# Kernel tuning notes

Hardware: AMD Instinct MI355X
Metric: run time of the kernel (lower is better)

## Reference

```python
import jax, jax.numpy as jnp
import numpy as np
import math

B, T, D_MODEL, N_HEAD = 2, 2048, 1024, 16
NUM_BUCKETS, MAX_DIST = 32, 128
D_HEAD = D_MODEL // N_HEAD


def _relative_position_bucket(rel_pos, num_buckets=NUM_BUCKETS, max_distance=MAX_DIST):
    # bidirectional=True branch of the torch code
    nb = num_buckets // 2
    buckets = (rel_pos > 0).astype(jnp.int32) * nb
    rel_pos = jnp.abs(rel_pos)
    max_exact = nb // 2
    is_small = rel_pos < max_exact
    # guard log(0); masked out by is_small anyway
    large = max_exact + (
        jnp.log(jnp.maximum(rel_pos, 1).astype(jnp.float32) / max_exact)
        / math.log(max_distance / max_exact) * (nb - max_exact)
    ).astype(jnp.int32)
    large = jnp.minimum(large, nb - 1)
    return buckets + jnp.where(is_small, rel_pos, large)


def compute_bias(rel_bias, q_len, kv_len):
    qp = jnp.arange(q_len, dtype=jnp.int32)[:, None]
    kp = jnp.arange(kv_len, dtype=jnp.int32)[None, :]
    buckets = _relative_position_bucket(kp - qp)          # [Tq, Tkv]
    vals = rel_bias[buckets]                              # [Tq, Tkv, H]
    return jnp.transpose(vals, (2, 0, 1))                 # [H, Tq, Tkv]


def setup_inputs() -> dict:
    key = jax.random.key(0)
    ks = jax.random.split(key, 9)
    inp = {
        'q': jax.random.normal(ks[0], (B, T, D_MODEL), jnp.float32),
        'k': jax.random.normal(ks[1], (B, T, D_MODEL), jnp.float32),
        'v': jax.random.normal(ks[2], (B, T, D_MODEL), jnp.float32),
        'mask': jax.random.randint(ks[3], (B, T, T), 0, 2, jnp.int32),
        'Wq': jax.random.normal(ks[4], (D_MODEL, D_MODEL), jnp.float32) * 0.02,
        'Wk': jax.random.normal(ks[5], (D_MODEL, D_MODEL), jnp.float32) * 0.02,
        'Wv': jax.random.normal(ks[6], (D_MODEL, D_MODEL), jnp.float32) * 0.02,
        'Wfc': jax.random.normal(ks[7], (D_MODEL, D_MODEL), jnp.float32) * 0.02,
        'rel_bias': jax.random.normal(ks[8], (NUM_BUCKETS, N_HEAD), jnp.float32) * 0.02,
    }
    return inp


def reference(q, k, v, mask, Wq, Wk, Wv, Wfc, rel_bias):
    b, tq, _ = q.shape
    tkv = k.shape[1]
    qh = (q @ Wq).reshape(b, tq, N_HEAD, D_HEAD)
    kh = (k @ Wk).reshape(b, tkv, N_HEAD, D_HEAD)
    vh = (v @ Wv).reshape(b, tkv, N_HEAD, D_HEAD)
    attn = jnp.einsum('blhd,bthd->bhlt', qh, kh) / np.sqrt(D_HEAD).astype(np.float32)
    position_bias = compute_bias(rel_bias, tq, tkv)       # [H, Tq, Tkv]
    attn = attn + position_bias[None]                     # broadcast over batch
    attn = jnp.where(mask[:, None] == 0, -1e9, attn)
    attn = jax.nn.softmax(attn, axis=-1)                  # dropout: eval mode (identity)
    out = jnp.einsum('bhlt,bthd->blhd', attn, vh).reshape(b, tq, D_MODEL)
    out = out @ Wfc
    return out, position_bias[:, None]                    # bias returned as [H,1,Tq,Tkv] like torch
```

## Files before the change

### kernel.cpp

```cpp
#include <hip/hip_runtime.h>
#include <math.h>

#define TT 2048
#define BB 2
#define HH 16
#define DMODEL 1024
#define NREL 4095

typedef __attribute__((ext_vector_type(8)))  _Float16 half8;
typedef __attribute__((ext_vector_type(4)))  _Float16 half4;
typedef __attribute__((ext_vector_type(16))) float    f32x16;
typedef __attribute__((ext_vector_type(4)))  int      int4v;

__device__ __forceinline__ f32x16 zero16() {
    f32x16 v;
#pragma unroll
    for (int i = 0; i < 16; ++i) v[i] = 0.f;
    return v;
}

__device__ __forceinline__ unsigned pkh(float a, float b) {
    union { _Float16 h[2]; unsigned u; } x;
    x.h[0] = (_Float16)a; x.h[1] = (_Float16)b;
    return x.u;
}

__device__ __forceinline__ void gload16(const void* g, void* l) {
    __builtin_amdgcn_global_load_lds(
        (const __attribute__((address_space(1))) void*)g,
        (__attribute__((address_space(3))) void*)l, 16, 0, 0);
}

__device__ __forceinline__ int rel_bucket(int rel) {
    int base = rel > 0 ? 16 : 0;
    int r = rel < 0 ? -rel : rel;
    int lb;
    if (r < 8)       lb = r;
    else if (r < 12) lb = 8;
    else if (r < 16) lb = 9;
    else if (r < 23) lb = 10;
    else if (r < 32) lb = 11;
    else if (r < 46) lb = 12;
    else if (r < 64) lb = 13;
    else if (r < 91) lb = 14;
    else             lb = 15;
    return base + lb;
}

__global__ __launch_bounds__(256) void prep_kernel(
    const float* __restrict__ q, const float* __restrict__ k,
    const float* __restrict__ v, const int* __restrict__ mask,
    const float* __restrict__ W0, const float* __restrict__ W1,
    const float* __restrict__ W2, const float* __restrict__ W3,
    const float* __restrict__ rel_bias,
    _Float16* __restrict__ q16, _Float16* __restrict__ k16,
    _Float16* __restrict__ v16, _Float16* __restrict__ WT,
    float* __restrict__ btable, unsigned* __restrict__ mb)
{
    __shared__ float t[64][65];
    int bid = blockIdx.x, tid = threadIdx.x;
    if (bid < 256) {
        int idx = bid * 256 + tid;
        if (idx < HH * NREL) {
            int h = idx / NREL, ri = idx % NREL;
            btable[idx] = rel_bias[rel_bucket(ri - (TT - 1)) * HH + h];
        }
    } else if (bid < 1280) {
        int zz = (bid - 256) >> 8, inner = (bid - 256) & 255;
        const float* src = zz == 0 ? W0 : zz == 1 ? W1 : zz == 2 ? W2 : W3;
        _Float16* dst = WT + (size_t)zz * DMODEL * DMODEL;
        int k0 = (inner >> 4) * 64, n0 = (inner & 15) * 64;
        int r = tid >> 4, c4 = (tid & 15) * 4;
#pragma unroll
        for (int i = 0; i < 4; ++i) {
            float4 vv = *(const float4*)(src + (size_t)(k0 + r + 16 * i) * DMODEL + n0 + c4);
            t[r + 16 * i][c4] = vv.x; t[r + 16 * i][c4 + 1] = vv.y;
            t[r + 16 * i][c4 + 2] = vv.z; t[r + 16 * i][c4 + 3] = vv.w;
        }
        __syncthreads();
        int rn = tid >> 2, ck = (tid & 3) * 16;
        half8 h0, h1;
#pragma unroll
        for (int j = 0; j < 8; ++j) h0[j] = (_Float16)t[ck + j][rn];
#pragma unroll
        for (int j = 0; j < 8; ++j) h1[j] = (_Float16)t[ck + 8 + j][rn];
        *(half8*)(dst + (size_t)(n0 + rn) * DMODEL + k0 + ck) = h0;
        *(half8*)(dst + (size_t)(n0 + rn) * DMODEL + k0 + ck + 8) = h1;
    } else if (bid < 7424) {
        int zz = (bid - 1280) >> 11, inner = (bid - 1280) & 2047;
        const float* src = zz == 0 ? q : zz == 1 ? k : v;
        _Float16* dst = zz == 0 ? q16 : zz == 1 ? k16 : v16;
        int i = inner * 256 + tid;
        const float4* in4 = (const float4*)src;
        float4 v0 = in4[(size_t)i * 2], v1 = in4[(size_t)i * 2 + 1];
        half8 h = {(_Float16)v0.x, (_Float16)v0.y, (_Float16)v0.z, (_Float16)v0.w,
                   (_Float16)v1.x, (_Float16)v1.y, (_Float16)v1.z, (_Float16)v1.w};
        *(half8*)(dst + (size_t)i * 8) = h;
    } else {
        int g = (bid - 7424) * 256 + tid;
        int vv = mask[g];
        unsigned long long bal = __ballot(vv != 0);
        if ((g & 63) == 0) {
            int word = g >> 5;
            mb[word]     = (unsigned)bal;
            mb[word + 1] = (unsigned)(bal >> 32);
        }
    }
}

__global__ __launch_bounds__(256) void gemm_proj3(
    const _Float16* __restrict__ q16, const _Float16* __restrict__ k16,
    const _Float16* __restrict__ v16, const _Float16* __restrict__ WT,
    _Float16* __restrict__ qhf, _Float16* __restrict__ khf,
    _Float16* __restrict__ vtf, int zbase)
{
    __shared__ __align__(16) char lds[65536];
    int z = zbase + blockIdx.z;
    const _Float16* A  = z == 0 ? q16 : z == 1 ? k16 : v16;
    const _Float16* Bt = WT + (size_t)z * DMODEL * DMODEL;
    int bm = blockIdx.x * 128, bn = blockIdx.y * 128;
    int tid = threadIdx.x;
    int wv = tid >> 6, lane = tid & 63, lo = lane & 31, hi = lane >> 5;
    int wr = wv >> 1, wc = wv & 1;
    int srow = wv * 32 + (lane >> 3);
    int scol = (lane & 7) * 8;
    const _Float16* Abase = A  + (size_t)(bm + srow) * DMODEL + scol;
    const _Float16* Bbase = Bt + (size_t)(bn + srow) * DMODEL + scol;

    f32x16 acc[2][2];
    acc[0][0] = zero16(); acc[0][1] = zero16();
    acc[1][0] = zero16(); acc[1][1] = zero16();

    auto stage = [&](int buf, int kt) {
#pragma unroll
        for (int t = 0; t < 4; ++t) {
            gload16(Abase + (size_t)t * 8 * DMODEL + kt * 64, lds + buf + wv * 4096 + t * 1024);
            gload16(Bbase + (size_t)t * 8 * DMODEL + kt * 64, lds + buf + 16384 + wv * 4096 + t * 1024);
        }
    };
    auto compute = [&](int buf) {
#pragma unroll
        for (int kk = 0; kk < 4; ++kk) {
            int cs = 2 * kk + hi;
            half8 a[2], b[2];
#pragma unroll
            for (int i = 0; i < 2; ++i) {
                a[i] = *(const half8*)(lds + buf + (wr * 64 + i * 32 + lo) * 128 + cs * 16);
                b[i] = *(const half8*)(lds + buf + 16384 + (wc * 64 + i * 32 + lo) * 128 + cs * 16);
            }
            acc[0][0] = __builtin_amdgcn_mfma_f32_32x32x16_f16(a[0], b[0], acc[0][0], 0, 0, 0);
            acc[0][1] = __builtin_amdgcn_mfma_f32_32x32x16_f16(a[0], b[1], acc[0][1], 0, 0, 0);
            acc[1][0] = __builtin_amdgcn_mfma_f32_32x32x16_f16(a[1], b[0], acc[1][0], 0, 0, 0);
            acc[1][1] = __builtin_amdgcn_mfma_f32_32x32x16_f16(a[1], b[1], acc[1][1], 0, 0, 0);
        }
    };

    stage(0, 0);
    __syncthreads();
    for (int kt = 0; kt < 16; kt += 2) {
        stage(32768, kt + 1);
        compute(0);
        __syncthreads();
        stage(0, kt + 2 < 16 ? kt + 2 : 15);
        compute(32768);
        __syncthreads();
    }

    if (z < 2) {
        _Float16* C = z == 0 ? qhf : khf;
#pragma unroll
        for (int j = 0; j < 2; ++j) {
            int n = bn + wc * 64 + j * 32 + lo;
            int h = n >> 6, d = n & 63;
#pragma unroll
            for (int i = 0; i < 2; ++i) {
                int mb2 = bm + wr * 64 + i * 32 + 4 * hi;
#pragma unroll
                for (int r = 0; r < 16; ++r) {
                    int m = mb2 + (r & 3) + 8 * (r >> 2);
                    int b = m >> 11, t = m & (TT - 1);
                    C[((size_t)(b * HH + h) * TT + t) * 64 + d] = (_Float16)acc[i][j][r];
                }
            }
        }
    } else {
#pragma unroll
        for (int j = 0; j < 2; ++j) {
            int n = bn + wc * 64 + j * 32 + lo;
            int h = n >> 6, d = n & 63;
#pragma unroll
            for (int i = 0; i < 2; ++i) {
                int mb2 = bm + wr * 64 + i * 32 + 4 * hi;
                int b = mb2 >> 11, tb = mb2 & (TT - 1);
#pragma unroll
                for (int r4 = 0; r4 < 4; ++r4) {
                    half4 hv = {(_Float16)acc[i][j][4 * r4 + 0], (_Float16)acc[i][j][4 * r4 + 1],
                                (_Float16)acc[i][j][4 * r4 + 2], (_Float16)acc[i][j][4 * r4 + 3]};
                    *(half4*)(vtf + ((size_t)(b * HH + h) * 64 + d) * TT + tb + 8 * r4) = hv;
                }
            }
        }
    }
}

__global__ __launch_bounds__(256) void attn_mfma(
    const _Float16* __restrict__ qh, const _Float16* __restrict__ kh,
    const _Float16* __restrict__ vt, const unsigned* __restrict__ maskbits,
    const float* __restrict__ btable, _Float16* __restrict__ Oout)
{
    int bid = blockIdx.x;
    int xcd = bid & 7, j = bid >> 3;
    int qt = j & 15, bh = xcd + 8 * (j >> 4);
    int h = bh & 15, b = bh >> 4;
    int tid = threadIdx.x;
    int wv = tid >> 6, lane = tid & 63, lo = lane & 31, hi = lane >> 5;
    int q0 = qt * 128 + wv * 32;

    const size_t bhoff = (size_t)(b * HH + h);
    const _Float16* Q = qh + (bhoff * TT + q0) * 64;
    const _Float16* K = kh + bhoff * TT * 64;
    const _Float16* V = vt + bhoff * 64 * TT;

    half8 qf[4];
#pragma unroll
    for (int c = 0; c < 4; ++c)
        qf[c] = *(const half8*)(Q + (size_t)lo * 64 + c * 16 + hi * 8);

    const float* bt = btable + h * NREL + (TT - 1) - (q0 + lo) + 4 * hi;
    const float bias_l = btable[h * NREL];
    const float bias_r = btable[h * NREL + NREL - 1];
    const unsigned* mw = maskbits + ((size_t)b * TT + q0 + lo) * 64;

    f32x16 acco0 = zero16(), acco1 = zero16();
    float m = -INFINITY, l = 0.f;

    for (int kt = 0; kt < TT / 64; ++kt) {
        int k0 = kt * 64;
        half8 kf[2][4];
#pragma unroll
        for (int g = 0; g < 2; ++g)
#pragma unroll
            for (int c = 0; c < 4; ++c)
                kf[g][c] = *(const half8*)(K + (size_t)(k0 + 32 * g + lo) * 64 + c * 16 + hi * 8);
        unsigned wm0 = mw[2 * kt], wm1 = mw[2 * kt + 1];

        f32x16 accs0 = zero16(), accs1 = zero16();
        __builtin_amdgcn_s_setprio(1);
#pragma unroll
        for (int c = 0; c < 4; ++c) {
            accs0 = __builtin_amdgcn_mfma_f32_32x32x16_f16(kf[0][c], qf[c], accs0, 0, 0, 0);
            accs1 = __builtin_amdgcn_mfma_f32_32x32x16_f16(kf[1][c], qf[c], accs1, 0, 0, 0);
        }
        __builtin_amdgcn_s_setprio(0);

        unsigned ws0 = wm0 >> (hi * 4), ws1 = wm1 >> (hi * 4);
        bool rconst = k0 > q0 + 121;
        bool lconst = k0 + 63 < q0 - 90;
        if (rconst | lconst) {
            float bc = rconst ? bias_r : bias_l;
#pragma unroll
            for (int r = 0; r < 16; ++r) {
                int sh = (r & 3) + 8 * (r >> 2);
                float s0 = fmaf(accs0[r], 0.125f, bc);
                float s1 = fmaf(accs1[r], 0.125f, bc);
                accs0[r] = ((ws0 >> sh) & 1) ? s0 : -1e9f;
                accs1[r] = ((ws1 >> sh) & 1) ? s1 : -1e9f;
            }
        } else {
#pragma unroll
            for (int r = 0; r < 16; ++r) {
                int sh = (r & 3) + 8 * (r >> 2);
                float s0 = fmaf(accs0[r], 0.125f, bt[k0 + sh]);
                float s1 = fmaf(accs1[r], 0.125f, bt[k0 + sh + 32]);
                accs0[r] = ((ws0 >> sh) & 1) ? s0 : -1e9f;
                accs1[r] = ((ws1 >> sh) & 1) ? s1 : -1e9f;
            }
        }

        float tm = accs0[0];
#pragma unroll
        for (int r = 1; r < 16; ++r) tm = fmaxf(tm, accs0[r]);
#pragma unroll
        for (int r = 0; r < 16; ++r) tm = fmaxf(tm, accs1[r]);
        tm = fmaxf(tm, __shfl_xor(tm, 32));
        float mnew = fmaxf(m, tm);
        float corr = __expf(m - mnew);
        float rs = 0.f;
#pragma unroll
        for (int r = 0; r < 16; ++r) {
            accs0[r] = __expf(accs0[r] - mnew); rs += accs0[r];
        }
#pragma unroll
        for (int r = 0; r < 16; ++r) {
            accs1[r] = __expf(accs1[r] - mnew); rs += accs1[r];
        }
        rs += __shfl_xor(rs, 32);
        l = l * corr + rs; m = mnew;
#pragma unroll
        for (int r = 0; r < 16; ++r) { acco0[r] *= corr; acco1[r] *= corr; }

        half8 vf[2][4];
#pragma unroll
        for (int dg = 0; dg < 2; ++dg)
#pragma unroll
            for (int c = 0; c < 4; ++c)
                vf[dg][c] = *(const half8*)(V + (size_t)(32 * dg + lo) * TT + k0 + c * 16 + hi * 8);

        half8 pb[4];
#pragma unroll
        for (int g = 0; g < 2; ++g)
#pragma unroll
            for (int hc = 0; hc < 2; ++hc) {
                int r0 = hc * 8;
                float p0 = g ? accs1[r0 + 0] : accs0[r0 + 0];
                float p1 = g ? accs1[r0 + 1] : accs0[r0 + 1];
                float p2 = g ? accs1[r0 + 2] : accs0[r0 + 2];
                float p3 = g ? accs1[r0 + 3] : accs0[r0 + 3];
                float p4 = g ? accs1[r0 + 4] : accs0[r0 + 4];
                float p5 = g ? accs1[r0 + 5] : accs0[r0 + 5];
                float p6 = g ? accs1[r0 + 6] : accs0[r0 + 6];
                float p7 = g ? accs1[r0 + 7] : accs0[r0 + 7];
                unsigned w0 = pkh(p0, p1);
                unsigned w2 = pkh(p4, p5);
                asm("v_permlane32_swap_b32 %0, %1" : "+v"(w0), "+v"(w2));
                unsigned w1 = pkh(p2, p3);
                unsigned w3 = pkh(p6, p7);
                asm("v_permlane32_swap_b32 %0, %1" : "+v"(w1), "+v"(w3));
                union { int4v i; half8 hf; } cv;
                cv.i = (int4v){(int)w0, (int)w1, (int)w2, (int)w3};
                pb[2 * g + hc] = cv.hf;
            }

        __builtin_amdgcn_s_setprio(1);
#pragma unroll
        for (int c = 0; c < 4; ++c) {
            acco0 = __builtin_amdgcn_mfma_f32_32x32x16_f16(vf[0][c], pb[c], acco0, 0, 0, 0);
            acco1 = __builtin_amdgcn_mfma_f32_32x32x16_f16(vf[1][c], pb[c], acco1, 0, 0, 0);
        }
        __builtin_amdgcn_s_setprio(0);
    }

    float inv = 1.f / l;
    _Float16* op = Oout + (bhoff * TT + q0 + lo) * 64;
#pragma unroll
    for (int r4 = 0; r4 < 4; ++r4) {
        int d0 = 8 * r4 + 4 * hi;
        half4 h0 = {(_Float16)(acco0[4 * r4 + 0] * inv), (_Float16)(acco0[4 * r4 + 1] * inv),
                    (_Float16)(acco0[4 * r4 + 2] * inv), (_Float16)(acco0[4 * r4 + 3] * inv)};
        *(half4*)(op + d0) = h0;
        half4 h1 = {(_Float16)(acco1[4 * r4 + 0] * inv), (_Float16)(acco1[4 * r4 + 1] * inv),
                    (_Float16)(acco1[4 * r4 + 2] * inv), (_Float16)(acco1[4 * r4 + 3] * inv)};
        *(half4*)(op + d0 + 32) = h1;
    }
}

__global__ __launch_bounds__(256) void fc_bias_kernel(
    const _Float16* __restrict__ O, const _Float16* __restrict__ Bt,
    float* __restrict__ out0, const float* __restrict__ btable,
    float* __restrict__ out1)
{
    __shared__ __align__(16) char lds[65536];
    int bid = blockIdx.x, tid = threadIdx.x;
    if (bid >= 256) {
        const int n4 = HH * TT * TT / 4, stride = 2048 * 256;
        for (int i4 = (bid - 256) * 256 + tid; i4 < n4; i4 += stride) {
            int i = i4 * 4;
            int kk = i & (TT - 1);
            int qq = (i >> 11) & (TT - 1);
            int hh2 = i >> 22;
            const float* btp = btable + hh2 * NREL + (kk - qq + (TT - 1));
            float4 vv = make_float4(btp[0], btp[1], btp[2], btp[3]);
            reinterpret_cast<float4*>(out1)[i4] = vv;
        }
        return;
    }
    int bm = (bid & 31) * 128, bn = (bid >> 5) * 128;
    int wv = tid >> 6, lane = tid & 63, lo = lane & 31, hi = lane >> 5;
    int wr = wv >> 1, wc = wv & 1;
    int srow = wv * 32 + (lane >> 3);
    int scol = (lane & 7) * 8;
    int bb = bm >> 11, tbase = bm & (TT - 1);
    const _Float16* Abase = O + ((size_t)(bb * HH) * TT + tbase + srow) * 64 + scol;
    const _Float16* Bbase = Bt + (size_t)(bn + srow) * DMODEL + scol;

    f32x16 acc[2][2];
    acc[0][0] = zero16(); acc[0][1] = zero16();
    acc[1][0] = zero16(); acc[1][1] = zero16();

    auto stage = [&](int buf, int kt) {
#pragma unroll
        for (int t = 0; t < 4; ++t) {
            gload16(Abase + (size_t)kt * TT * 64 + (size_t)t * 8 * 64, lds + buf + wv * 4096 + t * 1024);
            gload16(Bbase + (size_t)t * 8 * DMODEL + kt * 64, lds + buf + 16384 + wv * 4096 + t * 1024);
        }
    };
    auto compute = [&](int buf) {
#pragma unroll
        for (int kk = 0; kk < 4; ++kk) {
            int cs = 2 * kk + hi;
            half8 a[2], b[2];
#pragma unroll
            for (int i = 0; i < 2; ++i) {
                a[i] = *(const half8*)(lds + buf + (wr * 64 + i * 32 + lo) * 128 + cs * 16);
                b[i] = *(const half8*)(lds + buf + 16384 + (wc * 64 + i * 32 + lo) * 128 + cs * 16);
            }
            acc[0][0] = __builtin_amdgcn_mfma_f32_32x32x16_f16(a[0], b[0], acc[0][0], 0, 0, 0);
            acc[0][1] = __builtin_amdgcn_mfma_f32_32x32x16_f16(a[0], b[1], acc[0][1], 0, 0, 0);
            acc[1][0] = __builtin_amdgcn_mfma_f32_32x32x16_f16(a[1], b[0], acc[1][0], 0, 0, 0);
            acc[1][1] = __builtin_amdgcn_mfma_f32_32x32x16_f16(a[1], b[1], acc[1][1], 0, 0, 0);
        }
    };

    stage(0, 0);
    __syncthreads();
    for (int kt = 0; kt < 16; kt += 2) {
        stage(32768, kt + 1);
        compute(0);
        __syncthreads();
        stage(0, kt + 2 < 16 ? kt + 2 : 15);
        compute(32768);
        __syncthreads();
    }

#pragma unroll
    for (int j = 0; j < 2; ++j) {
        int n = bn + wc * 64 + j * 32 + lo;
#pragma unroll
        for (int i = 0; i < 2; ++i) {
            int mb2 = bm + wr * 64 + i * 32 + 4 * hi;
#pragma unroll
            for (int r = 0; r < 16; ++r) {
                int m = mb2 + (r & 3) + 8 * (r >> 2);
                out0[(size_t)m * DMODEL + n] = acc[i][j][r];
            }
        }
    }
}

extern "C" void kernel_launch(void* const* d_in, const int* in_sizes, int n_in,
                              void* d_out, int out_size, void* d_ws, size_t ws_size,
                              hipStream_t stream) {
    const float* q        = (const float*)d_in[0];
    const float* k        = (const float*)d_in[1];
    const float* v        = (const float*)d_in[2];
    const int*   mask     = (const int*)  d_in[3];
    const float* Wq       = (const float*)d_in[4];
    const float* Wk       = (const float*)d_in[5];
    const float* Wv       = (const float*)d_in[6];
    const float* Wfc      = (const float*)d_in[7];
    const float* rel_bias = (const float*)d_in[8];

    float* out0 = (float*)d_out;
    float* out1 = out0 + (size_t)BB * TT * DMODEL;

    char* w = (char*)d_ws;
    _Float16* q16 = (_Float16*)(w);
    _Float16* k16 = (_Float16*)(w + ((size_t)8  << 20));
    _Float16* v16 = (_Float16*)(w + ((size_t)16 << 20));
    _Float16* qhf = (_Float16*)(w + ((size_t)24 << 20));
    _Float16* khf = (_Float16*)(w + ((size_t)32 << 20));
    _Float16* WT  = (_Float16*)(w + ((size_t)40 << 20));
    float*    btable = (float*)(w + ((size_t)48 << 20));
    unsigned* mbits  = (unsigned*)(w + ((size_t)48 << 20) + ((size_t)1 << 19));
    bool big = ws_size >= ((size_t)58 << 20);
    _Float16* vtf = big ? (_Float16*)(w + ((size_t)49 << 20) + ((size_t)1 << 19))
                        : k16;
    _Float16* O = q16;

    prep_kernel<<<dim3(40192), dim3(256), 0, stream>>>(
        q, k, v, mask, Wq, Wk, Wv, Wfc, rel_bias, q16, k16, v16, WT, btable, mbits);

    if (big) {
        gemm_proj3<<<dim3(32, 8, 3), dim3(256), 0, stream>>>(q16, k16, v16, WT,
                                                             qhf, khf, vtf, 0);
    } else {
        gemm_proj3<<<dim3(32, 8, 1), dim3(256), 0, stream>>>(q16, k16, v16, WT, qhf, khf, vtf, 0);
        gemm_proj3<<<dim3(32, 8, 1), dim3(256), 0, stream>>>(q16, k16, v16, WT, qhf, khf, vtf, 1);
        gemm_proj3<<<dim3(32, 8, 1), dim3(256), 0, stream>>>(q16, k16, v16, WT, qhf, khf, vtf, 2);
    }

    attn_mfma<<<dim3(BB * HH * 16), dim3(256), 0, stream>>>(
        qhf, khf, vtf, mbits, btable, O);

    fc_bias_kernel<<<dim3(2304), dim3(256), 0, stream>>>(
        O, WT + (size_t)3 * DMODEL * DMODEL, out0, btable, out1);
}
```

Before: 284.9 us.

## Split attention KV range in two with a combine kernel

The attention kernel now takes a template split count. With the large workspace it launches twice as many blocks, and each block covers half of the key range. Each half writes its partial output plus row max and sum, and a new combine kernel merges the two halves with log-sum-exp weights. The aim is more blocks per CU and better latency hiding. The cost is an extra kernel launch and extra traffic for the partial outputs. The max and sum reductions are also rewritten as trees to shorten dependency chains, and launch bounds now request 4 blocks per CU.

Result: slower. 403.3 us (+41.6%).

```diff
diff --git a/kernel.cpp b/kernel.cpp
--- a/kernel.cpp
+++ b/kernel.cpp
@@ -120,7 +120,8 @@
     const _Float16* Bt = WT + (size_t)z * DMODEL * DMODEL;
     int bm = blockIdx.x * 128, bn = blockIdx.y * 128;
     int tid = threadIdx.x;
-    int wv = tid >> 6, lane = tid & 63, lo = lane & 31, hi = lane >> 5;
+    int wv = tid >> 6, lane = tid & 63, hi = lane >> 5;
+    int lo = lane & 31;
     int wr = wv >> 1, wc = wv & 1;
     int srow = wv * 32 + (lane >> 3);
     int scol = (lane & 7) * 8;
@@ -203,14 +204,20 @@
     }
 }
 
-__global__ __launch_bounds__(256) void attn_mfma(
+template<int NSPLIT>
+__global__ __launch_bounds__(256, 4) void attn_mfma(
     const _Float16* __restrict__ qh, const _Float16* __restrict__ kh,
     const _Float16* __restrict__ vt, const unsigned* __restrict__ maskbits,
-    const float* __restrict__ btable, _Float16* __restrict__ Oout)
+    const float* __restrict__ btable, _Float16* __restrict__ Oout,
+    float* __restrict__ ml)
 {
     int bid = blockIdx.x;
-    int xcd = bid & 7, j = bid >> 3;
-    int qt = j & 15, bh = xcd + 8 * (j >> 4);
+    int j = bid >> 3;
+    int qt = j & 15;
+    int sp, grp;
+    if (NSPLIT == 2) { sp = (j >> 4) & 1; grp = j >> 5; }
+    else             { sp = 0;            grp = j >> 4; }
+    int bh = (bid & 7) + 8 * grp;
     int h = bh & 15, b = bh >> 4;
     int tid = threadIdx.x;
     int wv = tid >> 6, lane = tid & 63, lo = lane & 31, hi = lane >> 5;
@@ -234,7 +241,8 @@
     f32x16 acco0 = zero16(), acco1 = zero16();
     float m = -INFINITY, l = 0.f;
 
-    for (int kt = 0; kt < TT / 64; ++kt) {
+    const int ktb = sp * (32 / NSPLIT);
+    for (int kt = ktb; kt < ktb + 32 / NSPLIT; ++kt) {
         int k0 = kt * 64;
         half8 kf[2][4];
 #pragma unroll
@@ -277,25 +285,30 @@
             }
         }
 
-        float tm = accs0[0];
-#pragma unroll
-        for (int r = 1; r < 16; ++r) tm = fmaxf(tm, accs0[r]);
-#pragma unroll
-        for (int r = 0; r < 16; ++r) tm = fmaxf(tm, accs1[r]);
+        float tr[8];
+#pragma unroll
+        for (int r = 0; r < 8; ++r)
+            tr[r] = fmaxf(fmaxf(accs0[r], accs0[r + 8]), fmaxf(accs1[r], accs1[r + 8]));
+#pragma unroll
+        for (int r = 0; r < 4; ++r) tr[r] = fmaxf(tr[r], tr[r + 4]);
+        float tm = fmaxf(fmaxf(tr[0], tr[1]), fmaxf(tr[2], tr[3]));
         tm = fmaxf(tm, __shfl_xor(tm, 32));
         float mnew = fmaxf(m, tm);
         float corr = __expf(m - mnew);
-        float rs = 0.f;
-#pragma unroll
-        for (int r = 0; r < 16; ++r) {
-            accs0[r] = __expf(accs0[r] - mnew); rs += accs0[r];
-        }
-#pragma unroll
-        for (int r = 0; r < 16; ++r) {
-            accs1[r] = __expf(accs1[r] - mnew); rs += accs1[r];
-        }
+        m = mnew;
+
+#pragma unroll
+        for (int r = 0; r < 16; ++r) accs0[r] = __expf(accs0[r] - m);
+#pragma unroll
+        for (int r = 0; r < 16; ++r) accs1[r] = __expf(accs1[r] - m);
+#pragma unroll
+        for (int r = 0; r < 8; ++r)
+            tr[r] = (accs0[r] + accs0[r + 8]) + (accs1[r] + accs1[r + 8]);
+#pragma unroll
+        for (int r = 0; r < 4; ++r) tr[r] += tr[r + 4];
+        float rs = (tr[0] + tr[1]) + (tr[2] + tr[3]);
         rs += __shfl_xor(rs, 32);
-        l = l * corr + rs; m = mnew;
+        l = l * corr + rs;
 #pragma unroll
         for (int r = 0; r < 16; ++r) { acco0[r] *= corr; acco1[r] *= corr; }
 
@@ -341,7 +354,7 @@
     }
 
     float inv = 1.f / l;
-    _Float16* op = Oout + (bhoff * TT + q0 + lo) * 64;
+    _Float16* op = Oout + (size_t)sp * (BB * HH * TT * 64) + (bhoff * TT + q0 + lo) * 64;
 #pragma unroll
     for (int r4 = 0; r4 < 4; ++r4) {
         int d0 = 8 * r4 + 4 * hi;
@@ -352,6 +365,32 @@
                     (_Float16)(acco1[4 * r4 + 2] * inv), (_Float16)(acco1[4 * r4 + 3] * inv)};
         *(half4*)(op + d0 + 32) = h1;
     }
+    if (NSPLIT == 2 && hi == 0) {
+        int row = (int)(bhoff * TT) + q0 + lo;
+        ml[sp * 131072 + row]         = m;
+        ml[sp * 131072 + 65536 + row] = l;
+    }
+}
+
+__global__ __launch_bounds__(256) void combine_kernel(
+    const _Float16* __restrict__ Ohalf, const float* __restrict__ ml,
+    _Float16* __restrict__ O)
+{
+    int idx = blockIdx.x * 256 + threadIdx.x;
+    int row = idx >> 3, d8 = (idx & 7) * 8;
+    float m0 = ml[row],          l0 = ml[65536 + row];
+    float m1 = ml[131072 + row], l1 = ml[196608 + row];
+    float mm = fmaxf(m0, m1);
+    float w0 = __expf(m0 - mm) * l0, w1 = __expf(m1 - mm) * l1;
+    float dn = fmaxf(w0 + w1, 1e-30f);
+    float c0 = w0 / dn, c1 = w1 / dn;
+    half8 a = *(const half8*)(Ohalf + (size_t)row * 64 + d8);
+    half8 b = *(const half8*)(Ohalf + (size_t)(BB * HH * TT * 64) + (size_t)row * 64 + d8);
+    half8 o;
+#pragma unroll
+    for (int jj = 0; jj < 8; ++jj)
+        o[jj] = (_Float16)(c0 * (float)a[jj] + c1 * (float)b[jj]);
+    *(half8*)(O + (size_t)row * 64 + d8) = o;
 }
 
 __global__ __launch_bounds__(256) void fc_bias_kernel(
@@ -465,7 +504,9 @@
     bool big = ws_size >= ((size_t)58 << 20);
     _Float16* vtf = big ? (_Float16*)(w + ((size_t)49 << 20) + ((size_t)1 << 19))
                         : k16;
-    _Float16* O = q16;
+    _Float16* Ohalf = (_Float16*)w;
+    float*    ml    = (float*)(w + ((size_t)40 << 20));
+    _Float16* O     = v16;
 
     prep_kernel<<<dim3(40192), dim3(256), 0, stream>>>(
         q, k, v, mask, Wq, Wk, Wv, Wfc, rel_bias, q16, k16, v16, WT, btable, mbits);
@@ -473,14 +514,16 @@
     if (big) {
         gemm_proj3<<<dim3(32, 8, 3), dim3(256), 0, stream>>>(q16, k16, v16, WT,
                                                              qhf, khf, vtf, 0);
+        attn_mfma<2><<<dim3(BB * HH * 16 * 2), dim3(256), 0, stream>>>(
+            qhf, khf, vtf, mbits, btable, Ohalf, ml);
+        combine_kernel<<<dim3(2048), dim3(256), 0, stream>>>(Ohalf, ml, O);
     } else {
         gemm_proj3<<<dim3(32, 8, 1), dim3(256), 0, stream>>>(q16, k16, v16, WT, qhf, khf, vtf, 0);
         gemm_proj3<<<dim3(32, 8, 1), dim3(256), 0, stream>>>(q16, k16, v16, WT, qhf, khf, vtf, 1);
         gemm_proj3<<<dim3(32, 8, 1), dim3(256), 0, stream>>>(q16, k16, v16, WT, qhf, khf, vtf, 2);
-    }
-
-    attn_mfma<<<dim3(BB * HH * 16), dim3(256), 0, stream>>>(
-        qhf, khf, vtf, mbits, btable, O);
+        attn_mfma<1><<<dim3(BB * HH * 16), dim3(256), 0, stream>>>(
+            qhf, khf, vtf, mbits, btable, O, ml);
+    }
 
     fc_bias_kernel<<<dim3(2304), dim3(256), 0, stream>>>(
         O, WT + (size_t)3 * DMODEL * DMODEL, out0, btable, out1);
```
